# Performance work log

Measured on AMD Instinct MI355X. Metric: run time of the kernel, lower is better.

The kernel has to match this reference:

```python
import jax, jax.numpy as jnp
import numpy as np

# dims: batch, history P, horizon Q, hidden D, nodes N, cells C=H*W, Z channels
B_, P_, Q_, D_, N_, C_, H_, W_, CZ = 16, 12, 12, 64, 2000, 1024, 32, 32, 2
K_DIFF = 3  # max diffusion step of DCGRUCell -> K+1 Chebyshev terms


def _mlp2(x, w1, b1, w2, b2):
    return jax.nn.relu(x @ w1 + b1) @ w2 + b2


def _st_embedding(SE, TE, sw1, sb1, sw2, sb2, tw1, tb1, tw2, tb2):
    # GMAN-style spatio-temporal embedding: SE (M,D), TE (B,P,2) ints
    se = _mlp2(SE, sw1, sb1, sw2, sb2)                                  # (M, D)
    te = jnp.concatenate([jax.nn.one_hot(TE[..., 0], 7, dtype=SE.dtype),
                          jax.nn.one_hot(TE[..., 1], 288, dtype=SE.dtype)], axis=-1)
    te = _mlp2(te, tw1, tb1, tw2, tb2)                                  # (B, P, D)
    return se[None, None] + te[:, :, None, :]                           # (B, P, M, D)


def _scaled_laplacian(adj):
    # DCRNN 'laplacian' filter: L_tilde = 2 L / lambda_max - I, lambda_max ~= 2
    A = jnp.maximum(adj, adj.T)
    d = A.sum(axis=1)
    dinv = jnp.where(d > 0, jax.lax.rsqrt(d), 0.0)
    eye = jnp.eye(A.shape[0], dtype=A.dtype)
    L = eye - (dinv[:, None] * A) * dinv[None, :]
    return L - eye


def _gconv(x, L, K):
    # Chebyshev diffusion features: x (B,N,F) -> (B,N,F*(K+1))
    xs = [x, jnp.einsum('nm,bmf->bnf', L, x)]
    for _ in range(2, K + 1):
        xs.append(2.0 * jnp.einsum('nm,bmf->bnf', L, xs[-1]) - xs[-2])
    b, n, f = x.shape
    return jnp.stack(xs, axis=-1).reshape(b, n, f * (K + 1))


def _hard_sigmoid(x):
    return jnp.clip(0.2 * x + 0.5, 0.0, 1.0)


def _conv2d(x, w):
    return jax.lax.conv_general_dilated(x, w, (1, 1), 'SAME',
        dimension_numbers=('NHWC', 'HWIO', 'NHWC'))


def _forward(X, Z, TE, adj_gg, adj_gr, gumbel_noise, se_x, se_z, movement_logits,
             stex_se_w1, stex_se_b1, stex_se_w2, stex_se_b2,
             stex_te_w1, stex_te_b1, stex_te_w2, stex_te_b2,
             stez_se_w1, stez_se_b1, stez_se_w2, stez_se_b2,
             stez_te_w1, stez_te_b1, stez_te_w2, stez_te_b2,
             fcs_z_w1, fcs_z_b1, fcs_z_w2, fcs_z_b2,
             fcs_x_in_w1, fcs_x_in_b1, fcs_x_in_w2, fcs_x_in_b2,
             mov_fc_w, mov_fc_b,
             fcs_x_out_w1, fcs_x_out_b1, fcs_x_out_w2, fcs_x_out_b2,
             convlstm_wx, convlstm_wh,
             dcgru_gate_w, dcgru_gate_b, dcgru_cand_w, dcgru_cand_b):
    B = X.shape[0]
    TEp = TE.astype(jnp.int32)[:, :P_, :]
    # --- cell branch ---
    STEZ = _st_embedding(se_z, TEp, stez_se_w1, stez_se_b1, stez_se_w2, stez_se_b2,
                         stez_te_w1, stez_te_b1, stez_te_w2, stez_te_b2)
    Zf = _mlp2(Z, fcs_z_w1, fcs_z_b1, fcs_z_w2, fcs_z_b2) + STEZ          # (B,P,C,D)
    Zg = Zf.reshape(B, P_, H_, W_, D_)
    def clstm_step(carry, x):
        h, c = carry
        gates = _conv2d(x, convlstm_wx) + _conv2d(h, convlstm_wh)         # (B,H,W,4D)
        i, f, g, o = jnp.split(gates, 4, axis=-1)
        c = _hard_sigmoid(f) * c + _hard_sigmoid(i) * jnp.tanh(g)
        h = _hard_sigmoid(o) * jnp.tanh(c)
        return (h, c), h
    hc0 = (jnp.zeros((B, H_, W_, D_), X.dtype), jnp.zeros((B, H_, W_, D_), X.dtype))
    _, hs = jax.lax.scan(clstm_step, hc0, jnp.swapaxes(Zg, 0, 1))
    Zc = jnp.swapaxes(hs, 0, 1).reshape(B, P_, C_, D_)
    # gumbel-softmax routing over cells (soft, tau=1)
    g = -jnp.log(-jnp.log(gumbel_noise + 1e-20) + 1e-20)
    mZ = jax.nn.softmax(movement_logits + g, axis=-1)                     # (C,C)
    Zc = jnp.einsum('cd,bpdk->bpck', mZ, Zc)
    Zc = jax.nn.relu(Zc @ mov_fc_w + mov_fc_b)
    ZX = jnp.einsum('nc,bpck->bpnk', adj_gr, Zc)                          # (B,P,N,D)
    # --- node branch ---
    STEX = _st_embedding(se_x, TEp, stex_se_w1, stex_se_b1, stex_se_w2, stex_se_b2,
                         stex_te_w1, stex_te_b1, stex_te_w2, stex_te_b2)
    Xf = _mlp2(X[..., None], fcs_x_in_w1, fcs_x_in_b1, fcs_x_in_w2, fcs_x_in_b2) + STEX + ZX
    L = _scaled_laplacian(adj_gg)
    def dcgru_step(h, x):
        xh = jnp.concatenate([x, h], axis=-1)                             # (B,N,2D)
        ru = jax.nn.sigmoid(_gconv(xh, L, K_DIFF) @ dcgru_gate_w + dcgru_gate_b)
        r, u = jnp.split(ru, 2, axis=-1)
        cnd = jnp.tanh(_gconv(jnp.concatenate([x, r * h], axis=-1), L, K_DIFF)
                       @ dcgru_cand_w + dcgru_cand_b)
        return u * h + (1.0 - u) * cnd, None
    h_last, _ = jax.lax.scan(dcgru_step, jnp.zeros((B, N_, D_), X.dtype),
                             jnp.swapaxes(Xf, 0, 1))                      # (B,N,D)
    Y = _mlp2(h_last, fcs_x_out_w1, fcs_x_out_b1, fcs_x_out_w2, fcs_x_out_b2)  # (B,N,Q)
    return jnp.transpose(Y, (0, 2, 1))                                    # (B,Q,N)


def setup_inputs() -> dict:
    key = jax.random.key(0)
    ks = iter(jax.random.split(key, 64))
    def rn(shape, s=0.05):
        return jax.random.normal(next(ks), shape, dtype=jnp.float32) * s
    def ru(shape):
        return jax.random.uniform(next(ks), shape, dtype=jnp.float32)
    z = lambda *s: jnp.zeros(s, jnp.float32)
    NM = K_DIFF + 1
    inp = {
        'X': rn((B_, P_, N_), 1.0),
        'Z': rn((B_, P_, C_, CZ), 1.0),
        'TE': jax.random.randint(next(ks), (B_, P_ + Q_, 2), 0, 7, dtype=jnp.int32),
        'adj_gg': ru((N_, N_)),
        'adj_gr': ru((N_, C_)) * 0.01,
        'gumbel_noise': jnp.clip(ru((C_, C_)), 1e-6, 1.0 - 1e-6),
        'se_x': rn((N_, D_)), 'se_z': rn((C_, D_)),
        'movement_logits': rn((C_, C_)),
        'stex_se_w1': rn((D_, D_)), 'stex_se_b1': z(D_), 'stex_se_w2': rn((D_, D_)), 'stex_se_b2': z(D_),
        'stex_te_w1': rn((295, D_)), 'stex_te_b1': z(D_), 'stex_te_w2': rn((D_, D_)), 'stex_te_b2': z(D_),
        'stez_se_w1': rn((D_, D_)), 'stez_se_b1': z(D_), 'stez_se_w2': rn((D_, D_)), 'stez_se_b2': z(D_),
        'stez_te_w1': rn((295, D_)), 'stez_te_b1': z(D_), 'stez_te_w2': rn((D_, D_)), 'stez_te_b2': z(D_),
        'fcs_z_w1': rn((CZ, D_)), 'fcs_z_b1': z(D_), 'fcs_z_w2': rn((D_, D_)), 'fcs_z_b2': z(D_),
        'fcs_x_in_w1': rn((1, D_)), 'fcs_x_in_b1': z(D_), 'fcs_x_in_w2': rn((D_, D_)), 'fcs_x_in_b2': z(D_),
        'mov_fc_w': rn((D_, D_)), 'mov_fc_b': z(D_),
        'fcs_x_out_w1': rn((D_, D_)), 'fcs_x_out_b1': z(D_), 'fcs_x_out_w2': rn((D_, Q_)), 'fcs_x_out_b2': z(Q_),
        'convlstm_wx': rn((3, 3, D_, 4 * D_)), 'convlstm_wh': rn((3, 3, D_, 4 * D_)),
        'dcgru_gate_w': rn((2 * D_ * NM, 2 * D_)), 'dcgru_gate_b': z(2 * D_),
        'dcgru_cand_w': rn((2 * D_ * NM, D_)), 'dcgru_cand_b': z(D_),
    }
    return inp


def reference(X, Z, TE, adj_gg, adj_gr, gumbel_noise, se_x, se_z, movement_logits,
              stex_se_w1, stex_se_b1, stex_se_w2, stex_se_b2,
              stex_te_w1, stex_te_b1, stex_te_w2, stex_te_b2,
              stez_se_w1, stez_se_b1, stez_se_w2, stez_se_b2,
              stez_te_w1, stez_te_b1, stez_te_w2, stez_te_b2,
              fcs_z_w1, fcs_z_b1, fcs_z_w2, fcs_z_b2,
              fcs_x_in_w1, fcs_x_in_b1, fcs_x_in_w2, fcs_x_in_b2,
              mov_fc_w, mov_fc_b,
              fcs_x_out_w1, fcs_x_out_b1, fcs_x_out_w2, fcs_x_out_b2,
              convlstm_wx, convlstm_wh,
              dcgru_gate_w, dcgru_gate_b, dcgru_cand_w, dcgru_cand_b):
    return _forward(X, Z, TE, adj_gg, adj_gr, gumbel_noise, se_x, se_z, movement_logits,
                    stex_se_w1, stex_se_b1, stex_se_w2, stex_se_b2,
                    stex_te_w1, stex_te_b1, stex_te_w2, stex_te_b2,
                    stez_se_w1, stez_se_b1, stez_se_w2, stez_se_b2,
                    stez_te_w1, stez_te_b1, stez_te_w2, stez_te_b2,
                    fcs_z_w1, fcs_z_b1, fcs_z_w2, fcs_z_b2,
                    fcs_x_in_w1, fcs_x_in_b1, fcs_x_in_w2, fcs_x_in_b2,
                    mov_fc_w, mov_fc_b,
                    fcs_x_out_w1, fcs_x_out_b1, fcs_x_out_w2, fcs_x_out_b2,
                    convlstm_wx, convlstm_wh,
                    dcgru_gate_w, dcgru_gate_b, dcgru_cand_w, dcgru_cand_b)
```

## Files before the change

kernel.cpp:

```cpp
#include <hip/hip_runtime.h>
#include <hip/hip_bf16.h>
#include <math.h>

typedef _Float16 fp16;
typedef _Float16 f16x8 __attribute__((ext_vector_type(8)));
typedef float f32x4 __attribute__((ext_vector_type(4)));

#define BB 16
#define PP 12
#define QQ 12
#define NN 2000
#define CC 1024
#define GP 34
#define GP2 1156

static __device__ __forceinline__ float ldf(float v) { return v; }
static __device__ __forceinline__ float ldf(fp16 v) { return (float)v; }
static __device__ __forceinline__ void stf(float* p, float v) { *p = v; }
static __device__ __forceinline__ void stf(fp16* p, float v) { *p = (fp16)v; }

static __device__ __forceinline__ void gload_lds16(const fp16* g, fp16* l) {
  __builtin_amdgcn_global_load_lds(
      (const __attribute__((address_space(1))) void*)g,
      (__attribute__((address_space(3))) void*)l, 16, 0, 0);
}


__global__ void k_f2h(fp16* __restrict__ dst, const float* __restrict__ src, long long n) {
  long long i = (long long)blockIdx.x * 256 + threadIdx.x;
  if (i < n) dst[i] = (fp16)src[i];
}

__global__ void k_wcatT(fp16* __restrict__ dst, const float* __restrict__ w39,
                        const float* __restrict__ w40) {
  int i = blockIdx.x * 256 + threadIdx.x;
  if (i >= 1152 * 256) return;
  int n = i & 255, kk = i >> 8;
  float v = (kk < 576) ? w39[kk * 256 + n] : w40[(kk - 576) * 256 + n];
  dst[(long long)n * 1152 + kk] = (fp16)v;
}

__global__ void k_gru_repackT(fp16* __restrict__ dst, const float* __restrict__ src, int O) {
  int i = blockIdx.x * 256 + threadIdx.x;
  if (i >= O * 512) return;
  int d = i >> 9;
  int kc = i & 511;
  int t = kc >> 7;
  int c = kc & 127;
  dst[i] = (fp16)src[(c * 4 + t) * O + d];
}

__global__ void k_w2T(fp16* __restrict__ dst, const float* __restrict__ src) {
  int i = blockIdx.x * 256 + threadIdx.x;
  if (i >= 4096) return;
  int d = i >> 6, k = i & 63;
  dst[i] = (fp16)src[k * 64 + d];
}

__global__ void k_dinv(const float* __restrict__ adj, float* __restrict__ dinv) {
  int row = blockIdx.x;
  float s = 0.f;
  for (int j = threadIdx.x; j < NN; j += 256)
    s += fmaxf(adj[(long long)row * NN + j], adj[(long long)j * NN + row]);
  __shared__ float red[256];
  red[threadIdx.x] = s;
  __syncthreads();
  for (int st = 128; st > 0; st >>= 1) {
    if (threadIdx.x < st) red[threadIdx.x] += red[threadIdx.x + st];
    __syncthreads();
  }
  if (threadIdx.x == 0) {
    float d = red[0];
    dinv[row] = d > 0.f ? 1.0f / sqrtf(d) : 0.f;
  }
}

__global__ void k_L(const float* __restrict__ adj, const float* __restrict__ dinv,
                    fp16* __restrict__ Lh) {
  long long i = (long long)blockIdx.x * 256 + threadIdx.x;
  if (i >= (long long)NN * NN) return;
  int r = (int)(i / NN), c = (int)(i % NN);
  float a = fmaxf(adj[(long long)r * NN + c], adj[(long long)c * NN + r]);
  Lh[(long long)r * 2048 + c] = (fp16)(-dinv[r] * a * dinv[c]);
}

__global__ void k_subdiag(fp16* __restrict__ M2) {
  int i = blockIdx.x * 256 + threadIdx.x;
  if (i >= NN) return;
  M2[(long long)i * 2048 + i] = (fp16)((float)M2[(long long)i * 2048 + i] - 1.0f);
}

__global__ void k_gumbel_softmax(const float* __restrict__ ml, const float* __restrict__ gn,
                                 fp16* __restrict__ mZ) {
  int row = blockIdx.x;
  __shared__ float buf[CC];
  __shared__ float red[256];
  int t = threadIdx.x;
  float mx = -1e30f;
  for (int j = t; j < CC; j += 256) {
    float u = gn[(long long)row * CC + j];
    float g = -logf(-logf(u + 1e-20f) + 1e-20f);
    float v = ml[(long long)row * CC + j] + g;
    buf[j] = v;
    mx = fmaxf(mx, v);
  }
  red[t] = mx;
  __syncthreads();
  for (int st = 128; st > 0; st >>= 1) {
    if (t < st) red[t] = fmaxf(red[t], red[t + st]);
    __syncthreads();
  }
  mx = red[0];
  __syncthreads();
  float s = 0.f;
  for (int j = t; j < CC; j += 256) {
    float e = expf(buf[j] - mx);
    buf[j] = e;
    s += e;
  }
  red[t] = s;
  __syncthreads();
  for (int st = 128; st > 0; st >>= 1) {
    if (t < st) red[t] += red[t + st];
    __syncthreads();
  }
  float inv = 1.0f / red[0];
  for (int j = t; j < CC; j += 256) mZ[(long long)row * CC + j] = (fp16)(buf[j] * inv);
}

__global__ void k_te(const int* __restrict__ TE, const float* __restrict__ w1,
                     const float* __restrict__ b1, float* __restrict__ tmp) {
  int i = blockIdx.x * 256 + threadIdx.x;
  if (i >= BB * PP * 64) return;
  int j = i & 63;
  int bp = i >> 6;
  int b = bp / PP, p = bp % PP;
  int te0 = TE[(b * (PP + QQ) + p) * 2 + 0];
  int te1 = TE[(b * (PP + QQ) + p) * 2 + 1];
  float v = w1[te0 * 64 + j] + w1[(7 + te1) * 64 + j] + b1[j];
  tmp[i] = fmaxf(v, 0.f);
}

__global__ void k_addb(float* __restrict__ dst, const float* __restrict__ b, int n) {
  int i = blockIdx.x * 256 + threadIdx.x;
  if (i < n) dst[i] += b[i & 63];
}

__global__ void k_zf1(const float* __restrict__ Z, const float* __restrict__ w1,
                      const float* __restrict__ b1, fp16* __restrict__ tmp) {
  long long i = (long long)blockIdx.x * 256 + threadIdx.x;
  if (i >= (long long)BB * PP * CC * 64) return;
  int j = (int)(i & 63);
  long long row = i >> 6;
  float v = Z[row * 2 + 0] * w1[j] + Z[row * 2 + 1] * w1[64 + j] + b1[j];
  tmp[i] = (fp16)fmaxf(v, 0.f);
}

__global__ void k_add_stez(fp16* __restrict__ dst, const fp16* __restrict__ src,
                           const float* __restrict__ seZ, const float* __restrict__ teZ) {
  long long i = (long long)blockIdx.x * 256 + threadIdx.x;
  if (i >= (long long)BB * PP * CC * 64) return;
  int j = (int)(i & 63);
  long long row = i >> 6;
  int c = (int)(row & 1023);
  int bp = (int)(row >> 10);
  int pc = ((c >> 5) + 1) * GP + (c & 31) + 1;
  dst[((long long)bp * GP2 + pc) * 64 + j] =
      (fp16)((float)src[i] + seZ[c * 64 + j] + teZ[bp * 64 + j]);
}

template <typename TA, typename TB, typename TC>
__global__ __launch_bounds__(256) void gemm_t(
    const TA* __restrict__ A, int lda, long long sA,
    const TB* __restrict__ Bm, int ldb, long long sB,
    TC* Cm, int ldc, long long sC,
    const TC* S, long long sS,
    const float* __restrict__ bias,
    int M, int Ncols, int K, float alpha, float beta, int act) {
  int bz = blockIdx.z;
  A += (long long)bz * sA;
  Bm += (long long)bz * sB;
  Cm += (long long)bz * sC;
  if (S) S += (long long)bz * sS;
  const int row0 = blockIdx.x * 64, col0 = blockIdx.y * 64;
  __shared__ float As[16][68];
  __shared__ float Bs[16][68];
  int tid = threadIdx.x, tx = tid & 15, ty = tid >> 4;
  float acc[4][4] = {};
  for (int k0 = 0; k0 < K; k0 += 16) {
#pragma unroll
    for (int j = 0; j < 4; ++j) {
      int e = tid + 256 * j;
      int m = e >> 4, kk = e & 15;
      int gm = row0 + m;
      As[kk][m] = (gm < M) ? ldf(A[(long long)gm * lda + k0 + kk]) : 0.f;
    }
#pragma unroll
    for (int j = 0; j < 4; ++j) {
      int e = tid + 256 * j;
      int kk = e >> 6, n = e & 63;
      int gn = col0 + n;
      Bs[kk][n] = (gn < Ncols) ? ldf(Bm[(long long)(k0 + kk) * ldb + gn]) : 0.f;
    }
    __syncthreads();
#pragma unroll
    for (int kk = 0; kk < 16; ++kk) {
      float a[4], bb[4];
#pragma unroll
      for (int i = 0; i < 4; ++i) a[i] = As[kk][ty * 4 + i];
#pragma unroll
      for (int j = 0; j < 4; ++j) bb[j] = Bs[kk][tx * 4 + j];
#pragma unroll
      for (int i = 0; i < 4; ++i)
#pragma unroll
        for (int j = 0; j < 4; ++j) acc[i][j] = fmaf(a[i], bb[j], acc[i][j]);
    }
    __syncthreads();
  }
#pragma unroll
  for (int i = 0; i < 4; ++i) {
    int r = row0 + ty * 4 + i;
    if (r >= M) continue;
#pragma unroll
    for (int j = 0; j < 4; ++j) {
      int cn = col0 + tx * 4 + j;
      if (cn >= Ncols) continue;
      float v = alpha * acc[i][j];
      if (bias) v += bias[cn];
      if (S) v += beta * ldf(S[(long long)r * ldc + cn]);
      if (act == 1) v = fmaxf(v, 0.f);
      else if (act == 2) v = 1.f / (1.f + expf(-v));
      else if (act == 3) v = tanhf(v);
      stf(&Cm[(long long)r * ldc + cn], v);
    }
  }
}

template <int MT, int MODE>
__global__ __launch_bounds__(256) void mfma7(
    const fp16* __restrict__ A,
    const fp16* __restrict__ U0base, long long uZ, int bHi,
    const fp16* __restrict__ xB, long long xZ,
    const fp16* __restrict__ Xc, long long XcSlab, int Xcld, int Xczmul,
    const fp16* __restrict__ Hc, long long HcSlab, int Hcld, int Hczmul,
    fp16* __restrict__ C, int ldc, long long cBatch,
    const float* __restrict__ bias,
    fp16* __restrict__ rhOut, const fp16* __restrict__ hIn,
    const fp16* __restrict__ uIn, long long uStride,
    int M, int Ncols) {
  __shared__ fp16 As[2][MT * 32];
  __shared__ fp16 Bs[2][64 * 32];
  const int z = blockIdx.z;
  const int n0 = blockIdx.y * 64;
  const fp16* U0z = U0base + (long long)z * uZ;
  const fp16* xBz = xB + (long long)z * xZ;
  C += (long long)z * cBatch;
  if (rhOut) rhOut += (long long)z * uZ;
  if (hIn) hIn += (long long)z * uZ;
  if (uIn) uIn += (long long)z * uStride;
  const int tid = threadIdx.x;
  const int lane = tid & 63, wv = tid >> 6;
  const int wr = wv >> 1, wc = wv & 1;
  const int quad = lane >> 4, ln = lane & 15;
  constexpr int WM = MT / 32;

  const fp16* aSrc[MT / 64];
#pragma unroll
  for (int i = 0; i < MT / 64; ++i) {
    int c = i * 256 + tid;
    int row = c >> 2;
    int lseg = (c & 3) ^ ((c >> 3) & 3);
    aSrc[i] = A + (long long)row * 512 + lseg * 8;
  }
  const int brow = tid >> 2;
  const int blseg = (tid & 3) ^ ((tid >> 3) & 3);
  const long long bnode = n0 + brow;

  f32x4 acc[WM][2];
#pragma unroll
  for (int i = 0; i < WM; ++i)
#pragma unroll
    for (int j = 0; j < 2; ++j) acc[i][j] = (f32x4){0.f, 0.f, 0.f, 0.f};

  auto stage = [&](int t, int buf) {
    const int k0 = t * 32;
#pragma unroll
    for (int i = 0; i < MT / 64; ++i)
      gload_lds16(aSrc[i] + k0, &As[buf][(i * 256 + tid) * 8]);
    if (k0 < 128) {
      int kin = k0 + (tid & 31);
      int ngrp = tid >> 5;
      int n = n0 + ngrp * 8;
      const fp16* src = (kin < 64) ? (xBz + (long long)kin * 2048 + n)
                                   : (U0z + (long long)(kin + bHi) * 2048 + n);
      f16x8 v = *(const f16x8*)src;
      int kk = tid & 31;
#pragma unroll
      for (int j = 0; j < 8; ++j) {
        int rn = ngrp * 8 + j;
        Bs[buf][rn * 32 + ((((kk >> 3) ^ ((rn >> 1) & 3)) << 3) | (kk & 7))] = v[j];
      }
    } else {
      int slab = k0 >> 7;
      int kin = (k0 & 127) + blseg * 8;
      const fp16* src;
      if (kin < 64)
        src = Xc + (long long)(slab - 1) * XcSlab + bnode * Xcld +
              (long long)z * Xczmul + kin;
      else
        src = Hc + (long long)(slab - 1) * HcSlab + bnode * Hcld +
              (long long)z * Hczmul + (kin - 64);
      gload_lds16(src, &Bs[buf][tid * 8]);
    }
  };

  const int sw = (quad ^ ((ln >> 1) & 3)) << 3;
  stage(0, 0);
  for (int t = 0; t < 16; ++t) {
    const int buf = t & 1;
    __syncthreads();
    if (t + 1 < 16) stage(t + 1, buf ^ 1);
    f16x8 af[WM], bf[2];
#pragma unroll
    for (int wm = 0; wm < WM; ++wm) {
      int row = wr * (MT / 2) + wm * 16 + ln;
      af[wm] = *(const f16x8*)&As[buf][row * 32 + sw];
    }
#pragma unroll
    for (int wn = 0; wn < 2; ++wn) {
      int row = wc * 32 + wn * 16 + ln;
      bf[wn] = *(const f16x8*)&Bs[buf][row * 32 + sw];
    }
#pragma unroll
    for (int wm = 0; wm < WM; ++wm)
#pragma unroll
      for (int wn = 0; wn < 2; ++wn)
        acc[wm][wn] =
            __builtin_amdgcn_mfma_f32_16x16x32_f16(af[wm], bf[wn], acc[wm][wn], 0, 0, 0);
  }
#pragma unroll
  for (int wm = 0; wm < WM; ++wm) {
#pragma unroll
    for (int wn = 0; wn < 2; ++wn) {
#pragma unroll
      for (int r = 0; r < 4; ++r) {
        int gm = wr * (MT / 2) + wm * 16 + quad * 4 + r;
        int gn = n0 + wc * 32 + wn * 16 + ln;
        if (gm < M && gn < Ncols) {
          float v = acc[wm][wn][r];
          v += bias[gm];
          if (MODE == 1) {
            v = 1.f / (1.f + expf(-v));
            C[(long long)gm * ldc + gn] = (fp16)v;
            if (gm < 64) {
              float h = (float)hIn[(long long)gm * 2048 + gn];
              rhOut[(long long)gm * 2048 + gn] = (fp16)(v * h);
            }
          } else {
            v = tanhf(v);
            float u = (float)uIn[(long long)(64 + gm) * NN + gn];
            long long ci = (long long)gm * ldc + gn;
            float h = (float)C[ci];
            C[ci] = (fp16)(u * h + (1.f - u) * v);
          }
        }
      }
    }
  }
}

template <int MT, int NT>
__global__ __launch_bounds__(256) void mfma3(
    const fp16* __restrict__ A, int lda, long long zA, int aMsh, long long aMslab,
    const fp16* __restrict__ B, int ldb, long long zB,
    fp16* __restrict__ C, int ldc, long long zC, int cMsh, long long cMslab, int cNsh,
    long long cNslab,
    const fp16* __restrict__ S, long long zS, float beta,
    const float* __restrict__ rowBias, long long zRB,
    const float* __restrict__ s2T, int s2ld,
    int M, int Ncols, int K, float alpha, int act) {
  __shared__ fp16 As[MT][40];
  __shared__ fp16 Bs[NT][40];
  const int z = blockIdx.z;
  const int gm0 = blockIdx.x * MT, n0 = blockIdx.y * NT;
  A += (long long)z * zA;
  B += (long long)z * zB;
  C += (long long)z * zC;
  if (S) S += (long long)z * zS;
  const int tid = threadIdx.x;
  const int lane = tid & 63, wv = tid >> 6;
  const int wr = wv >> 1, wc = wv & 1;
  const int quad = lane >> 4, ln = lane & 15;
  const unsigned aMmask = (1u << aMsh) - 1u;
  const unsigned cMmask = (1u << cMsh) - 1u;
  const unsigned cNmask = (1u << cNsh) - 1u;
  constexpr int WM = MT / 32, WN = NT / 32;
  f32x4 acc[WM][WN];
#pragma unroll
  for (int i = 0; i < WM; ++i)
#pragma unroll
    for (int j = 0; j < WN; ++j) acc[i][j] = (f32x4){0.f, 0.f, 0.f, 0.f};

  for (int k0 = 0; k0 < K; k0 += 32) {
#pragma unroll
    for (int i = 0; i < MT / 64; ++i) {
      int c = tid + 256 * i;
      int row = c >> 2, seg = c & 3;
      int gm = gm0 + row;
      int kk0 = k0 + seg * 8;
      const fp16* src = A + ((long long)((unsigned)gm >> aMsh)) * aMslab +
                        (long long)(gm & aMmask) * lda + kk0;
      if (gm < M && kk0 + 8 <= K) {
        *(f16x8*)&As[row][seg * 8] = *(const f16x8*)src;
      } else {
#pragma unroll
        for (int j = 0; j < 8; ++j)
          As[row][seg * 8 + j] = (gm < M && kk0 + j < K) ? src[j] : (fp16)0.f;
      }
    }
#pragma unroll
    for (int i = 0; i < NT / 64; ++i) {
      int c = tid + 256 * i;
      int n = c >> 2, seg = c & 3;
      int gn = n0 + n;
      int kk0 = k0 + seg * 8;
      const fp16* src = B + (long long)gn * ldb + kk0;
      if (gn < Ncols && kk0 + 8 <= K) {
        *(f16x8*)&Bs[n][seg * 8] = *(const f16x8*)src;
      } else {
#pragma unroll
        for (int j = 0; j < 8; ++j)
          Bs[n][seg * 8 + j] = (gn < Ncols && kk0 + j < K) ? src[j] : (fp16)0.f;
      }
    }
    __syncthreads();
    f16x8 af[WM], bf[WN];
#pragma unroll
    for (int wm = 0; wm < WM; ++wm)
      af[wm] = *(const f16x8*)&As[wr * (MT / 2) + wm * 16 + ln][quad * 8];
#pragma unroll
    for (int wn = 0; wn < WN; ++wn)
      bf[wn] = *(const f16x8*)&Bs[wc * (NT / 2) + wn * 16 + ln][quad * 8];
#pragma unroll
    for (int wm = 0; wm < WM; ++wm)
#pragma unroll
      for (int wn = 0; wn < WN; ++wn)
        acc[wm][wn] =
            __builtin_amdgcn_mfma_f32_16x16x32_f16(af[wm], bf[wn], acc[wm][wn], 0, 0, 0);
    __syncthreads();
  }
#pragma unroll
  for (int wm = 0; wm < WM; ++wm) {
#pragma unroll
    for (int wn = 0; wn < WN; ++wn) {
#pragma unroll
      for (int r = 0; r < 4; ++r) {
        int gm = gm0 + wr * (MT / 2) + wm * 16 + quad * 4 + r;
        int gn = n0 + wc * (NT / 2) + wn * 16 + ln;
        if (gm < M && gn < Ncols) {
          float v = alpha * acc[wm][wn][r];
          if (rowBias) v += rowBias[(long long)z * zRB + gm];
          if (s2T) v += s2T[(long long)gn * s2ld + gm];
          long long ci = ((long long)((unsigned)gm >> cMsh)) * cMslab +
                         (long long)(gm & cMmask) * ldc +
                         ((long long)((unsigned)gn >> cNsh)) * cNslab + (gn & cNmask);
          if (S) v += beta * (float)S[ci];
          if (act == 1) v = fmaxf(v, 0.f);
          else if (act == 2) v = 1.f / (1.f + expf(-v));
          else if (act == 3) v = tanhf(v);
          C[ci] = (fp16)v;
        }
// ... 84 lines not shown
      int row = wc * (NT / 2) + wn * 16 + ln;
      bf[wn] = *(const f16x8*)&Bs[buf][row * 32 + sw];
    }
#pragma unroll
    for (int wm = 0; wm < WM; ++wm)
#pragma unroll
      for (int wn = 0; wn < WN; ++wn)
        acc[wm][wn] =
            __builtin_amdgcn_mfma_f32_16x16x32_f16(af[wm], bf[wn], acc[wm][wn], 0, 0, 0);
  }
#pragma unroll
  for (int wm = 0; wm < WM; ++wm)
#pragma unroll
    for (int wn = 0; wn < WN; ++wn)
#pragma unroll
      for (int r = 0; r < 4; ++r) {
        int gm = gm0 + wr * (MT / 2) + wm * 16 + quad * 4 + r;
        int gn = n0 + wc * (NT / 2) + wn * 16 + ln;
        long long ci = ((long long)((unsigned)gm >> cMsh)) * cMslab +
                       (long long)(gm & cMmask) * ldc +
                       ((long long)((unsigned)gn >> cNsh)) * cNslab + (gn & cNmask);
        float v = alpha * acc[wm][wn][r];
        if (S) v += beta * (float)S[ci];
        C[ci] = (fp16)v;
      }
}

template <int MT, int NT>
__global__ __launch_bounds__(256) void mfma6(
    const fp16* __restrict__ A, int lda,
    const fp16* __restrict__ b0, const fp16* __restrict__ b1, int rsh, int ssh,
    long long z0, long long z1, int ldb,
    fp16* __restrict__ C, int ldc, int cMsh, long long cMslab,
    int K) {
  __shared__ fp16 As[2][MT * 32];
  __shared__ fp16 Bs[2][NT * 32];
  const int tid = threadIdx.x;
  const int gm0 = blockIdx.x * MT, n0 = blockIdx.y * NT;
  const unsigned cMmask = (1u << cMsh) - 1u;
  const int lane = tid & 63, wv = tid >> 6;
  const int wr = wv >> 1, wc = wv & 1;
  const int quad = lane >> 4, ln = lane & 15;
  constexpr int WM = MT / 32, WN = NT / 32;

  const fp16* aSrc[MT / 64];
  const fp16* bSrc[NT / 64];
#pragma unroll
  for (int i = 0; i < MT / 64; ++i) {
    int c = i * 256 + tid;
    int lseg = (c & 3) ^ ((c >> 3) & 3);
    aSrc[i] = A + (long long)(gm0 + (c >> 2)) * lda + lseg * 8;
  }
#pragma unroll
  for (int i = 0; i < NT / 64; ++i) {
    int c = i * 256 + tid;
    int lseg = (c & 3) ^ ((c >> 3) & 3);
    int gn = n0 + (c >> 2);
    unsigned b = (unsigned)gn >> rsh;
    unsigned wi = (unsigned)gn & ((1u << rsh) - 1u);
    unsigned sel = wi >> ssh;
    unsigned r = wi & ((1u << ssh) - 1u);
    const fp16* bb = sel ? (b1 + (long long)b * z1) : (b0 + (long long)b * z0);
    bSrc[i] = bb + (long long)r * ldb + lseg * 8;
  }

  f32x4 acc[WM][WN];
#pragma unroll
  for (int i = 0; i < WM; ++i)
#pragma unroll
    for (int j = 0; j < WN; ++j) acc[i][j] = (f32x4){0.f, 0.f, 0.f, 0.f};

  const int sw = (quad ^ ((ln >> 1) & 3)) << 3;

#pragma unroll
  for (int i = 0; i < MT / 64; ++i) gload_lds16(aSrc[i], &As[0][(i * 256 + tid) * 8]);
#pragma unroll
  for (int i = 0; i < NT / 64; ++i) gload_lds16(bSrc[i], &Bs[0][(i * 256 + tid) * 8]);

  const int nk = K >> 5;
  for (int t = 0; t < nk; ++t) {
    const int buf = t & 1;
    __syncthreads();
    if (t + 1 < nk) {
      const int k1 = (t + 1) * 32;
#pragma unroll
      for (int i = 0; i < MT / 64; ++i)
        gload_lds16(aSrc[i] + k1, &As[buf ^ 1][(i * 256 + tid) * 8]);
#pragma unroll
      for (int i = 0; i < NT / 64; ++i)
        gload_lds16(bSrc[i] + k1, &Bs[buf ^ 1][(i * 256 + tid) * 8]);
    }
    f16x8 af[WM], bf[WN];
#pragma unroll
    for (int wm = 0; wm < WM; ++wm) {
      int row = wr * (MT / 2) + wm * 16 + ln;
      af[wm] = *(const f16x8*)&As[buf][row * 32 + sw];
    }
#pragma unroll
    for (int wn = 0; wn < WN; ++wn) {
      int row = wc * (NT / 2) + wn * 16 + ln;
      bf[wn] = *(const f16x8*)&Bs[buf][row * 32 + sw];
    }
#pragma unroll
    for (int wm = 0; wm < WM; ++wm)
#pragma unroll
      for (int wn = 0; wn < WN; ++wn)
        acc[wm][wn] =
            __builtin_amdgcn_mfma_f32_16x16x32_f16(af[wm], bf[wn], acc[wm][wn], 0, 0, 0);
  }
#pragma unroll
  for (int wm = 0; wm < WM; ++wm)
#pragma unroll
    for (int wn = 0; wn < WN; ++wn)
#pragma unroll
      for (int r = 0; r < 4; ++r) {
        int gm = gm0 + wr * (MT / 2) + wm * 16 + quad * 4 + r;
        int gn = n0 + wc * (NT / 2) + wn * 16 + ln;
        long long ci = ((long long)((unsigned)gm >> cMsh)) * cMslab +
                       (long long)(gm & cMmask) * ldc + gn;
        C[ci] = (fp16)acc[wm][wn][r];
      }
}

__global__ __launch_bounds__(256) void k_zxtfin(
    const fp16* __restrict__ w2T, const fp16* __restrict__ Tmat,
    fp16* __restrict__ ZXt, const float* __restrict__ teXb, const float* __restrict__ seX) {
  __shared__ fp16 As[64][72];
  __shared__ fp16 Bs[128][72];
  const int z = blockIdx.z;
  const int n0 = blockIdx.y * 128;
  const fp16* Tz = Tmat + (long long)z * 2048 * 64;
  fp16* Cz = ZXt + (long long)z * 64 * 2048;
  const float* tb = teXb + z * 64;
  const int tid = threadIdx.x;
  const int lane = tid & 63, wv = tid >> 6;
  const int wr = wv >> 1, wc = wv & 1;
  const int quad = lane >> 4, ln = lane & 15;
#pragma unroll
  for (int i = 0; i < 2; ++i) {
    int c = tid + 256 * i;
    int row = c >> 3, seg = c & 7;
    *(f16x8*)&As[row][seg * 8] = *(const f16x8*)(w2T + row * 64 + seg * 8);
  }
#pragma unroll
  for (int i = 0; i < 4; ++i) {
    int c = tid + 256 * i;
    int row = c >> 3, seg = c & 7;
    *(f16x8*)&Bs[row][seg * 8] =
        *(const f16x8*)(Tz + (long long)(n0 + row) * 64 + seg * 8);
  }
  __syncthreads();
  f32x4 acc[2][4];
#pragma unroll
  for (int i = 0; i < 2; ++i)
#pragma unroll
    for (int j = 0; j < 4; ++j) acc[i][j] = (f32x4){0.f, 0.f, 0.f, 0.f};
#pragma unroll
  for (int kt = 0; kt < 2; ++kt) {
    f16x8 af[2], bf[4];
#pragma unroll
    for (int wm = 0; wm < 2; ++wm)
      af[wm] = *(const f16x8*)&As[wr * 32 + wm * 16 + ln][kt * 32 + quad * 8];
#pragma unroll
    for (int wn = 0; wn < 4; ++wn)
      bf[wn] = *(const f16x8*)&Bs[wc * 64 + wn * 16 + ln][kt * 32 + quad * 8];
#pragma unroll
    for (int wm = 0; wm < 2; ++wm)
#pragma unroll
      for (int wn = 0; wn < 4; ++wn)
        acc[wm][wn] =
            __builtin_amdgcn_mfma_f32_16x16x32_f16(af[wm], bf[wn], acc[wm][wn], 0, 0, 0);
  }
#pragma unroll
  for (int wm = 0; wm < 2; ++wm)
#pragma unroll
    for (int wn = 0; wn < 4; ++wn)
#pragma unroll
      for (int r = 0; r < 4; ++r) {
        int gm = wr * 32 + wm * 16 + quad * 4 + r;
        int gn = n0 + wc * 64 + wn * 16 + ln;
        long long ci = (long long)gm * 2048 + gn;
        float v = 0.f;
        if (gn < NN)
          v = acc[wm][wn][r] + (float)Cz[ci] + tb[gm] + seX[(long long)gn * 64 + gm];
        Cz[ci] = (fp16)v;
      }
}

__global__ __launch_bounds__(256) void k_conv4(
    const fp16* __restrict__ Zfp, const fp16* __restrict__ hp,
    const fp16* __restrict__ wcatT, fp16* __restrict__ gates, int p) {
  __shared__ fp16 As[2][128 * 32];
  __shared__ fp16 Bs[2][64 * 32];
  const int gm0 = blockIdx.x * 128, n0 = blockIdx.y * 64;
  const int tid = threadIdx.x;
  const int lane = tid & 63, wv = tid >> 6;
  const int wr = wv >> 1, wc = wv & 1;
  const int quad = lane >> 4, ln = lane & 15;

  long long aZ[2], aH[2];
#pragma unroll
  for (int i = 0; i < 2; ++i) {
    int c = tid + 256 * i;
    int row = c >> 2;
    int lseg = (c & 3) ^ ((c >> 3) & 3);
    int m = gm0 + row;
    int b = m >> 10, y = (m >> 5) & 31, x = m & 31;
    int pc = (y + 1) * GP + (x + 1);
    aZ[i] = ((long long)(b * PP + p) * GP2 + pc) * 64 + lseg * 8;
    aH[i] = ((long long)b * GP2 + pc) * 64 + lseg * 8;
  }
  const fp16* bBase;
  {
    int row = tid >> 2;
    int lseg = (tid & 3) ^ ((tid >> 3) & 3);
    bBase = wcatT + (long long)(n0 + row) * 1152 + lseg * 8;
  }
  f32x4 acc[4][2];
#pragma unroll
  for (int i = 0; i < 4; ++i)
#pragma unroll
    for (int j = 0; j < 2; ++j) acc[i][j] = (f32x4){0.f, 0.f, 0.f, 0.f};

  auto stage = [&](int t, int buf) {
    int tap = (t >> 1) % 9, half = t & 1;
    int srcsel = t >= 18;
    int off = ((tap / 3 - 1) * GP + (tap % 3 - 1)) * 64 + half * 32;
#pragma unroll
    for (int i = 0; i < 2; ++i) {
      const fp16* src = srcsel ? (hp + aH[i] + off) : (Zfp + aZ[i] + off);
      gload_lds16(src, &As[buf][(i * 256 + tid) * 8]);
    }
    gload_lds16(bBase + t * 32, &Bs[buf][tid * 8]);
  };
  stage(0, 0);
  const int sw = (quad ^ ((ln >> 1) & 3)) << 3;
  for (int t = 0; t < 36; ++t) {
    const int buf = t & 1;
    __syncthreads();
    if (t + 1 < 36) stage(t + 1, buf ^ 1);
    f16x8 af[4], bf[2];
#pragma unroll
    for (int wm = 0; wm < 4; ++wm) {
      int row = wr * 64 + wm * 16 + ln;
      af[wm] = *(const f16x8*)&As[buf][row * 32 + sw];
    }
#pragma unroll
    for (int wn = 0; wn < 2; ++wn) {
      int row = wc * 32 + wn * 16 + ln;
      bf[wn] = *(const f16x8*)&Bs[buf][row * 32 + sw];
    }
#pragma unroll
    for (int wm = 0; wm < 4; ++wm)
#pragma unroll
      for (int wn = 0; wn < 2; ++wn)
        acc[wm][wn] =
            __builtin_amdgcn_mfma_f32_16x16x32_f16(af[wm], bf[wn], acc[wm][wn], 0, 0, 0);
  }
#pragma unroll
  for (int wm = 0; wm < 4; ++wm)
#pragma unroll
    for (int wn = 0; wn < 2; ++wn)
#pragma unroll
      for (int r = 0; r < 4; ++r) {
        int gm = gm0 + wr * 64 + wm * 16 + quad * 4 + r;
        int gn = n0 + wc * 32 + wn * 16 + ln;
        gates[(long long)gm * 256 + gn] = (fp16)acc[wm][wn][r];
      }
}

__global__ void k_clstm_update(const fp16* __restrict__ gates, float* __restrict__ c,
                               fp16* __restrict__ h, fp16* __restrict__ ZclT, int p) {
  long long i = (long long)blockIdx.x * 256 + threadIdx.x;
  if (i >= (long long)BB * CC * 64) return;
  int d = (int)(i & 63);
  long long bc = i >> 6;
  int b = (int)(bc >> 10);
  int cell = (int)(bc & 1023);
  const fp16* g = gates + (((long long)b * CC) + cell) * 256;
  float gi = (float)g[d], gf = (float)g[64 + d], gg = (float)g[128 + d],
        go = (float)g[192 + d];
  float hs_f = fminf(fmaxf(0.2f * gf + 0.5f, 0.f), 1.f);
  float hs_i = fminf(fmaxf(0.2f * gi + 0.5f, 0.f), 1.f);
  float hs_o = fminf(fmaxf(0.2f * go + 0.5f, 0.f), 1.f);
  float cv = hs_f * c[i] + hs_i * tanhf(gg);
  c[i] = cv;
  float hv = hs_o * tanhf(cv);
  int pc = ((cell >> 5) + 1) * GP + (cell & 31) + 1;
  h[((long long)b * GP2 + pc) * 64 + d] = (fp16)hv;
  ZclT[(((long long)(b * PP + p)) * 64 + d) * CC + cell] = (fp16)hv;
}

__global__ void k_tmat(const float* __restrict__ X, const float* __restrict__ w1,
                       const float* __restrict__ b1, fp16* __restrict__ T, long long nrows) {
  long long i = (long long)blockIdx.x * 256 + threadIdx.x;
  if (i >= nrows * 64) return;
  int j = (int)(i & 63);
  long long row = i >> 6;
  int z = (int)(row / NN);
  int n = (int)(row - (long long)z * NN);
  T[(((long long)z * 2048) + n) * 64 + j] = (fp16)fmaxf(X[row] * w1[j] + b1[j], 0.f);
}

__global__ void k_trT(const fp16* __restrict__ U0, float* __restrict__ htmp) {
  long long i = (long long)blockIdx.x * 256 + threadIdx.x;
  if (i >= (long long)BB * NN * 64) return;
  int d = (int)(i & 63);
  long long bn = i >> 6;
  int b = (int)(bn / NN);
  int n = (int)(bn % NN);
  htmp[i] = (float)U0[((long long)b * 192 + 64 + d) * 2048 + n];
}

__global__ void k_out(const float* __restrict__ Y, float* __restrict__ out) {
  int i = blockIdx.x * 256 + threadIdx.x;
  if (i >= BB * QQ * NN) return;
  int n = i % NN;
  int bq = i / NN;
  int b = bq / QQ, q = bq % QQ;
  out[i] = Y[((long long)b * NN + n) * 12 + q];
}

template <typename TA, typename TB, typename TC>
static void launch_gemm(hipStream_t stream, const TA* A, int lda, long long sA,
                        const TB* Bm, int ldb, long long sB, TC* Cm, int ldc, long long sC,
                        const TC* S, long long sS, const float* bias, int M, int Nc, int K,
                        float alpha, float beta, int act, int batch) {
  dim3 g((M + 63) / 64, (Nc + 63) / 64, batch);
  gemm_t<TA, TB, TC><<<g, dim3(256), 0, stream>>>(A, lda, sA, Bm, ldb, sB, Cm, ldc, sC, S,
                                                  sS, bias, M, Nc, K, alpha, beta, act);
}

extern "C" void kernel_launch(void* const* d_in, const int* in_sizes, int n_in,
                              void* d_out, int out_size, void* d_ws, size_t ws_size,
                              hipStream_t stream) {
  char* base = (char*)d_ws;
  size_t off = 0;
  auto alloc_bytes = [&](size_t nb) -> char* {
    char* p = base + off;
    off += (nb + 255) & ~(size_t)255;
    return p;
  };
  auto allocf = [&](size_t n) -> float* { return (float*)alloc_bytes(n * 4); };
  auto alloch = [&](size_t n) -> fp16* { return (fp16*)alloc_bytes(n * 2); };

  const float* X = (const float*)d_in[0];
  const float* Z = (const float*)d_in[1];
  const int* TE = (const int*)d_in[2];
  const float* adj_gg = (const float*)d_in[3];
  const float* adj_gr = (const float*)d_in[4];
  const float* gumbel = (const float*)d_in[5];
  const float* se_x = (const float*)d_in[6];
  const float* se_z = (const float*)d_in[7];
  const float* movement = (const float*)d_in[8];
  auto W = [&](int i) { return (const float*)d_in[i]; };

  fp16* wcatT = alloch((size_t)256 * 1152);
  fp16* gwT = alloch(128 * 512);
  fp16* cwT = alloch(64 * 512);
  fp16* w2T = alloch(64 * 64);
  fp16* w2mT = alloch(64 * 64);
  float* dinv = allocf(NN);
  fp16* LMall = alloch((size_t)6144 * 2048);
  fp16* mZh = alloch((size_t)CC * CC);
  fp16* agh2 = alloch((size_t)2048 * CC);
  float* seZ = allocf(CC * 64);
  float* teZ = allocf(BB * PP * 64);
  float* seX = allocf(NN * 64);
  float* teXb = allocf(BB * PP * 64);
  float* mtmp = allocf(NN * 64);
  float* tetmp = allocf(BB * PP * 64);
  fp16* ruT = alloch((size_t)BB * 128 * NN);
  char* pool = alloc_bytes(50331648);
  fp16* Uall = (fp16*)pool;
  fp16* gates = (fp16*)pool;
  fp16* chh = (fp16*)(pool + 8388608);
  float* ccc = (float*)(pool + 12582912);
  fp16* Zmix = (fp16*)pool;
  fp16* ZmovT = (fp16*)(pool + 25165824);
  fp16* zpool = alloch((size_t)BB * PP * 64 * 2048);
  fp16* Zfp = zpool;
  fp16* ZXt = zpool;
  fp16* Zc = alloch((size_t)BB * PP * CC * 64);

  if (off > ws_size) return;

  const long long uB = 192LL * 2048;
  const long long USL = 16LL * uB;
  const long long ZXB = 12LL * 64 * 2048;
  fp16* Lh = LMall;
  fp16* M2h = LMall + 2048LL * 2048;
  fp16* M3h = LMall + 4096LL * 2048;
  const int KCH = 2016;

  k_wcatT<<<dim3(1152), dim3(256), 0, stream>>>(wcatT, W(39), W(40));
  k_gru_repackT<<<dim3(256), dim3(256), 0, stream>>>(gwT, W(41), 128);
  k_gru_repackT<<<dim3(128), dim3(256), 0, stream>>>(cwT, W(43), 64);
  k_w2T<<<dim3(16), dim3(256), 0, stream>>>(w2T, W(31));
  k_w2T<<<dim3(16), dim3(256), 0, stream>>>(w2mT, W(33));
  k_dinv<<<dim3(NN), dim3(256), 0, stream>>>(adj_gg, dinv);
  hipMemsetAsync(LMall, 0, (size_t)6144 * 2048 * 2, stream);
  k_L<<<dim3((NN * NN + 255) / 256), dim3(256), 0, stream>>>(adj_gg, dinv, Lh);
  mfma4<64, 128><<<dim3(32, 16, 1), dim3(256), 0, stream>>>(
      Lh, Lh, 31, 31, 0LL, 0LL, 2048, Lh, 2048, 0LL, M2h, 2048, 0LL, 31, 0LL, 31, 0LL,
      (const fp16*)nullptr, 2.f, 0.f, KCH);
  k_subdiag<<<dim3((NN + 255) / 256), dim3(256), 0, stream>>>(M2h);
  mfma4<64, 128><<<dim3(32, 16, 1), dim3(256), 0, stream>>>(
      Lh, Lh, 31, 31, 0LL, 0LL, 2048, M2h, 2048, 0LL, M3h, 2048, 0LL, 31, 0LL, 31, 0LL,
      (const fp16*)Lh, 2.f, -1.f, KCH);
  k_gumbel_softmax<<<dim3(CC), dim3(256), 0, stream>>>(movement, gumbel, mZh);
  k_f2h<<<dim3((NN * CC + 255) / 256), dim3(256), 0, stream>>>(agh2, adj_gr,
                                                               (long long)NN * CC);
  hipMemsetAsync(agh2 + (size_t)NN * CC, 0, (size_t)(2048 - NN) * CC * 2, stream);

  launch_gemm(stream, se_z, 64, 0LL, W(17), 64, 0LL, mtmp, 64, 0LL, (float*)nullptr, 0LL,
              W(18), CC, 64, 64, 1.f, 0.f, 1, 1);
  launch_gemm(stream, (const float*)mtmp, 64, 0LL, W(19), 64, 0LL, seZ, 64, 0LL,
              (float*)nullptr, 0LL, W(20), CC, 64, 64, 1.f, 0.f, 0, 1);
  k_te<<<dim3((BB * PP * 64 + 255) / 256), dim3(256), 0, stream>>>(TE, W(21), W(22), tetmp);
  launch_gemm(stream, (const float*)tetmp, 64, 0LL, W(23), 64, 0LL, teZ, 64, 0LL,
              (float*)nullptr, 0LL, W(24), BB * PP, 64, 64, 1.f, 0.f, 0, 1);
  launch_gemm(stream, se_x, 64, 0LL, W(9), 64, 0LL, mtmp, 64, 0LL, (float*)nullptr, 0LL,
              W(10), NN, 64, 64, 1.f, 0.f, 1, 1);
  launch_gemm(stream, (const float*)mtmp, 64, 0LL, W(11), 64, 0LL, seX, 64, 0LL,
              (float*)nullptr, 0LL, W(12), NN, 64, 64, 1.f, 0.f, 0, 1);
  k_te<<<dim3((BB * PP * 64 + 255) / 256), dim3(256), 0, stream>>>(TE, W(13), W(14), tetmp);
  launch_gemm(stream, (const float*)tetmp, 64, 0LL, W(15), 64, 0LL, teXb, 64, 0LL,
              (float*)nullptr, 0LL, W(16), BB * PP, 64, 64, 1.f, 0.f, 0, 1);
  k_addb<<<dim3((BB * PP * 64 + 255) / 256), dim3(256), 0, stream>>>(teXb, W(32),
                                                                     BB * PP * 64);

  long long nZ = (long long)BB * PP * CC * 64;
  k_zf1<<<dim3((int)((nZ + 255) / 256)), dim3(256), 0, stream>>>(Z, W(25), W(26), Zc);
  launch_gemm(stream, (const fp16*)Zc, 64, 0LL, W(27), 64, 0LL, (fp16*)pool, 64, 0LL,
              (fp16*)nullptr, 0LL, W(28), BB * PP * CC, 64, 64, 1.f, 0.f, 0, 1);
  hipMemsetAsync(zpool, 0, (size_t)BB * PP * GP2 * 64 * 2, stream);
  k_add_stez<<<dim3((int)((nZ + 255) / 256)), dim3(256), 0, stream>>>(Zfp, (fp16*)pool,
                                                                      seZ, teZ);

  hipMemsetAsync(chh, 0, (size_t)BB * GP2 * 64 * 2, stream);
  hipMemsetAsync(ccc, 0, (size_t)BB * CC * 64 * 4, stream);
  for (int p = 0; p < PP; ++p) {
    k_conv4<<<dim3(BB * CC / 128, 4), dim3(256), 0, stream>>>(Zfp, chh, wcatT, gates, p);
    k_clstm_update<<<dim3((int)(((long long)BB * CC * 64 + 255) / 256)), dim3(256), 0,
                     stream>>>(gates, ccc, chh, Zc, p);
  }

  mfma4<128, 64><<<dim3(8, 1, 192), dim3(256), 0, stream>>>(
      mZh, mZh, 31, 31, 0LL, 0LL, CC, (const fp16*)Zc, CC, (long long)64 * CC, Zmix, 64,
      (long long)CC * 64, 31, 0LL, 31, 0LL, (const fp16*)nullptr, 1.f, 0.f, CC);
  mfma3<64, 128><<<dim3(1, 8, 192), dim3(256), 0, stream>>>(
      w2mT, 64, 0LL, 31, 0LL, Zmix, 64, (long long)CC * 64, ZmovT, CC, (long long)64 * CC,
      31, 0LL, 31, 0LL, (const fp16*)nullptr, 0LL, 0.f, W(34), 0LL, nullptr, 0, 64, CC, 64,
      1.f, 1);

  mfma4<128, 128><<<dim3(96, 16, 1), dim3(256), 0, stream>>>(
      ZmovT, ZmovT, 31, 31, 0LL, 0LL, 1024, agh2, 1024, 0LL, ZXt, 2048, 0LL, 31, 0LL, 31,
      0LL, (const fp16*)nullptr, 1.f, 0.f, 1024);

  fp16* Tmat = Zc;
  for (int half = 0; half < 2; ++half) {
    long long z0 = 96LL * half;
    k_tmat<<<dim3((int)((96LL * NN * 64 + 255) / 256)), dim3(256), 0, stream>>>(
        X + z0 * NN, W(29), W(30), Tmat, 96LL * NN);
    k_zxtfin<<<dim3(1, 16, 96), dim3(256), 0, stream>>>(
        w2T, Tmat, ZXt + z0 * 64 * 2048, teXb + z0 * 64, seX);
  }

  fp16* U0 = Uall;
  fp16* Tn = Uall + USL;
  fp16* Tn2 = Uall + 3 * USL;
  const long long TnSlab = 2048LL * 2048;
  const long long Tn2Slab = 2048LL * 1024;
  hipMemsetAsync(U0, 0, (size_t)USL * 2, stream);

  for (int p = 0; p < PP; ++p) {
    const fp16* xP = ZXt + (long long)p * 64 * 2048;
    mfma6<128, 128><<<dim3(48, 16), dim3(256), 0, stream>>>(
        LMall, 2048, xP, U0 + 64 * 2048, 7, 6, ZXB, uB, 2048, Tn, 2048, 11, TnSlab, KCH);
    mfma7<128, 1><<<dim3(1, 32, BB), dim3(256), 0, stream>>>(
        gwT, U0, uB, 0, xP, ZXB,
        Tn, TnSlab, 2048, 128,
        Tn + 64, TnSlab, 2048, 128,
        ruT, NN, (long long)128 * NN, W(42), U0 + 128 * 2048, U0 + 64 * 2048,
        (const fp16*)nullptr, 0LL, 128, NN);
    mfma6<128, 128><<<dim3(48, 8), dim3(256), 0, stream>>>(
        LMall, 2048, U0 + 128 * 2048, U0 + 128 * 2048, 6, 6, uB, uB, 2048, Tn2, 1024, 11,
        Tn2Slab, KCH);
    mfma7<64, 2><<<dim3(1, 32, BB), dim3(256), 0, stream>>>(
        cwT, U0, uB, 64, xP, ZXB,
        Tn, TnSlab, 2048, 128,
        Tn2, Tn2Slab, 1024, 64,
        U0 + 64 * 2048, 2048, uB, W(44), (fp16*)nullptr, (const fp16*)nullptr,
        (const fp16*)ruT, (long long)128 * NN, 64, NN);
  }

  float* htmp = (float*)Zc;
  float* out1 = (float*)(Zc + 5120000);
  float* out2 = (float*)(Zc + 10240000);
  k_trT<<<dim3((int)(((long long)BB * NN * 64 + 255) / 256)), dim3(256), 0, stream>>>(U0,
                                                                                      htmp);
  launch_gemm(stream, (const float*)htmp, 64, 0LL, W(35), 64, 0LL, out1, 64, 0LL,
              (float*)nullptr, 0LL, W(36), BB * NN, 64, 64, 1.f, 0.f, 1, 1);
  launch_gemm(stream, (const float*)out1, 64, 0LL, W(37), 12, 0LL, out2, 12, 0LL,
              (float*)nullptr, 0LL, W(38), BB * NN, 12, 64, 1.f, 0.f, 0, 1);
  k_out<<<dim3((BB * QQ * NN + 255) / 256), dim3(256), 0, stream>>>(out2, (float*)d_out);
}
```

Before: 2.938 ms.

## Fuse Z second MLP layer with ST-embedding scatter and fuse output head into MFMA kernel

Result: no change. 2.908 ms (-1.0%).

```diff
diff --git a/kernel.cpp b/kernel.cpp
--- a/kernel.cpp
+++ b/kernel.cpp
@@ -55,6 +55,13 @@
   if (i >= 4096) return;
   int d = i >> 6, k = i & 63;
   dst[i] = (fp16)src[k * 64 + d];
+}
+
+__global__ void k_wT(fp16* __restrict__ dst, const float* __restrict__ src, int J, int JP) {
+  int i = blockIdx.x * 256 + threadIdx.x;
+  if (i >= JP * 64) return;
+  int j = i >> 6, k = i & 63;
+  dst[i] = (fp16)((j < J) ? src[k * J + j] : 0.f);
 }
 
 __global__ void k_dinv(const float* __restrict__ adj, float* __restrict__ dinv) {
@@ -156,17 +163,165 @@
   tmp[i] = (fp16)fmaxf(v, 0.f);
 }
 
-__global__ void k_add_stez(fp16* __restrict__ dst, const fp16* __restrict__ src,
-                           const float* __restrict__ seZ, const float* __restrict__ teZ) {
-  long long i = (long long)blockIdx.x * 256 + threadIdx.x;
-  if (i >= (long long)BB * PP * CC * 64) return;
-  int j = (int)(i & 63);
-  long long row = i >> 6;
-  int c = (int)(row & 1023);
-  int bp = (int)(row >> 10);
-  int pc = ((c >> 5) + 1) * GP + (c & 31) + 1;
-  dst[((long long)bp * GP2 + pc) * 64 + j] =
-      (fp16)((float)src[i] + seZ[c * 64 + j] + teZ[bp * 64 + j]);
+__global__ __launch_bounds__(256) void k_zf2(
+    const fp16* __restrict__ A, const fp16* __restrict__ w27T,
+    const float* __restrict__ b28, const float* __restrict__ seZ,
+    const float* __restrict__ teZ, fp16* __restrict__ Zfp) {
+  __shared__ fp16 As[128 * 64];
+  __shared__ fp16 Bs[64 * 64];
+  const int tid = threadIdx.x;
+  const int gm0 = blockIdx.x * 128;
+  const int lane = tid & 63, wv = tid >> 6;
+  const int wr = wv >> 1, wc = wv & 1;
+  const int quad = lane >> 4, ln = lane & 15;
+#pragma unroll
+  for (int i = 0; i < 4; ++i) {
+    int c = i * 256 + tid;
+    int row = c >> 3;
+    int lseg = (c & 7) ^ (row & 7);
+    gload_lds16(A + (long long)(gm0 + row) * 64 + lseg * 8, &As[c * 8]);
+  }
+#pragma unroll
+  for (int i = 0; i < 2; ++i) {
+    int c = i * 256 + tid;
+    int row = c >> 3;
+    int lseg = (c & 7) ^ (row & 7);
+    gload_lds16(w27T + (long long)row * 64 + lseg * 8, &Bs[c * 8]);
+  }
+  f32x4 acc[4][2];
+#pragma unroll
+  for (int i = 0; i < 4; ++i)
+#pragma unroll
+    for (int j = 0; j < 2; ++j) acc[i][j] = (f32x4){0.f, 0.f, 0.f, 0.f};
+  __syncthreads();
+#pragma unroll
+  for (int kt = 0; kt < 2; ++kt) {
+    f16x8 af[4], bf[2];
+#pragma unroll
+    for (int wm = 0; wm < 4; ++wm) {
+      int row = wr * 64 + wm * 16 + ln;
+      int slot = (kt * 4 + quad) ^ (row & 7);
+      af[wm] = *(const f16x8*)&As[row * 64 + slot * 8];
+    }
+#pragma unroll
+    for (int wn = 0; wn < 2; ++wn) {
+      int row = wc * 32 + wn * 16 + ln;
+      int slot = (kt * 4 + quad) ^ (row & 7);
+      bf[wn] = *(const f16x8*)&Bs[row * 64 + slot * 8];
+    }
+#pragma unroll
+    for (int wm = 0; wm < 4; ++wm)
+#pragma unroll
+      for (int wn = 0; wn < 2; ++wn)
+        acc[wm][wn] =
+            __builtin_amdgcn_mfma_f32_16x16x32_f16(af[wm], bf[wn], acc[wm][wn], 0, 0, 0);
+  }
+#pragma unroll
+  for (int wm = 0; wm < 4; ++wm)
+#pragma unroll
+    for (int wn = 0; wn < 2; ++wn)
+#pragma unroll
+      for (int r = 0; r < 4; ++r) {
+        int gm = gm0 + wr * 64 + wm * 16 + quad * 4 + r;
+        int j = wc * 32 + wn * 16 + ln;
+        int c = gm & 1023;
+        int bp = gm >> 10;
+        int pc = ((c >> 5) + 1) * GP + (c & 31) + 1;
+        Zfp[((long long)bp * GP2 + pc) * 64 + j] =
+            (fp16)(acc[wm][wn][r] + b28[j] + seZ[c * 64 + j] + teZ[bp * 64 + j]);
+      }
+}
+
+__global__ __launch_bounds__(256) void k_head(
+    const fp16* __restrict__ U0, const fp16* __restrict__ w35T,
+    const float* __restrict__ b36, const fp16* __restrict__ w37T,
+    const float* __restrict__ b38, float* __restrict__ out) {
+  __shared__ fp16 hT[128 * 72];
+  __shared__ fp16 Bs[64 * 64];
+  __shared__ fp16 h2[128 * 72];
+  const int b = blockIdx.y;
+  const int n0 = blockIdx.x * 128;
+  const int tid = threadIdx.x;
+  const int lane = tid & 63, wv = tid >> 6;
+  const int wr = wv >> 1, wc = wv & 1;
+  const int quad = lane >> 4, ln = lane & 15;
+  const fp16* hbase = U0 + ((long long)b * 192 + 64) * 2048;
+#pragma unroll
+  for (int i = 0; i < 4; ++i) {
+    int task = i * 256 + tid;
+    int d = task >> 4, ng = task & 15;
+    f16x8 v = *(const f16x8*)(hbase + (long long)d * 2048 + n0 + ng * 8);
+#pragma unroll
+    for (int k = 0; k < 8; ++k) hT[(ng * 8 + k) * 72 + d] = v[k];
+  }
+#pragma unroll
+  for (int i = 0; i < 2; ++i) {
+    int c = i * 256 + tid;
+    int row = c >> 3, s = c & 7;
+    *(f16x8*)&Bs[row * 64 + (s ^ (row & 7)) * 8] =
+        *(const f16x8*)(w35T + row * 64 + s * 8);
+  }
+  __syncthreads();
+  f32x4 a1[4][2];
+#pragma unroll
+  for (int i = 0; i < 4; ++i)
+#pragma unroll
+    for (int j = 0; j < 2; ++j) a1[i][j] = (f32x4){0.f, 0.f, 0.f, 0.f};
+#pragma unroll
+  for (int kt = 0; kt < 2; ++kt) {
+    f16x8 af[4], bf[2];
+#pragma unroll
+    for (int wm = 0; wm < 4; ++wm) {
+      int row = wr * 64 + wm * 16 + ln;
+      af[wm] = *(const f16x8*)&hT[row * 72 + kt * 32 + quad * 8];
+    }
+#pragma unroll
+    for (int wn = 0; wn < 2; ++wn) {
+      int row = wc * 32 + wn * 16 + ln;
+      int slot = (kt * 4 + quad) ^ (row & 7);
+      bf[wn] = *(const f16x8*)&Bs[row * 64 + slot * 8];
+    }
+#pragma unroll
+    for (int wm = 0; wm < 4; ++wm)
+#pragma unroll
+      for (int wn = 0; wn < 2; ++wn)
+        a1[wm][wn] =
+            __builtin_amdgcn_mfma_f32_16x16x32_f16(af[wm], bf[wn], a1[wm][wn], 0, 0, 0);
+  }
+#pragma unroll
+  for (int wm = 0; wm < 4; ++wm)
+#pragma unroll
+    for (int wn = 0; wn < 2; ++wn)
+#pragma unroll
+      for (int r = 0; r < 4; ++r) {
+        int rl = wr * 64 + wm * 16 + quad * 4 + r;
+        int j = wc * 32 + wn * 16 + ln;
+        h2[rl * 72 + j] = (fp16)fmaxf(a1[wm][wn][r] + b36[j], 0.f);
+      }
+  __syncthreads();
+  f32x4 a2[2];
+#pragma unroll
+  for (int i = 0; i < 2; ++i) a2[i] = (f32x4){0.f, 0.f, 0.f, 0.f};
+#pragma unroll
+  for (int kt = 0; kt < 2; ++kt) {
+    f16x8 bf = *(const f16x8*)(w37T + ln * 64 + kt * 32 + quad * 8);
+#pragma unroll
+    for (int wm = 0; wm < 2; ++wm) {
+      int row = wv * 32 + wm * 16 + ln;
+      f16x8 af = *(const f16x8*)&h2[row * 72 + kt * 32 + quad * 8];
+      a2[wm] = __builtin_amdgcn_mfma_f32_16x16x32_f16(af, bf, a2[wm], 0, 0, 0);
+    }
+  }
+#pragma unroll
+  for (int wm = 0; wm < 2; ++wm)
+#pragma unroll
+    for (int r = 0; r < 4; ++r) {
+      int nl = wv * 32 + wm * 16 + quad * 4 + r;
+      int n = n0 + nl;
+      int q = ln;
+      if (n < NN && q < 12)
+        out[((long long)b * 12 + q) * NN + n] = a2[wm][r] + b38[q];
+    }
 }
 
 template <typename TA, typename TB, typename TC>
@@ -857,25 +1012,6 @@
   T[(((long long)z * 2048) + n) * 64 + j] = (fp16)fmaxf(X[row] * w1[j] + b1[j], 0.f);
 }
 
-__global__ void k_trT(const fp16* __restrict__ U0, float* __restrict__ htmp) {
-  long long i = (long long)blockIdx.x * 256 + threadIdx.x;
-  if (i >= (long long)BB * NN * 64) return;
-  int d = (int)(i & 63);
-  long long bn = i >> 6;
-  int b = (int)(bn / NN);
-  int n = (int)(bn % NN);
-  htmp[i] = (float)U0[((long long)b * 192 + 64 + d) * 2048 + n];
-}
-
-__global__ void k_out(const float* __restrict__ Y, float* __restrict__ out) {
-  int i = blockIdx.x * 256 + threadIdx.x;
-  if (i >= BB * QQ * NN) return;
-  int n = i % NN;
-  int bq = i / NN;
-  int b = bq / QQ, q = bq % QQ;
-  out[i] = Y[((long long)b * NN + n) * 12 + q];
-}
-
 template <typename TA, typename TB, typename TC>
 static void launch_gemm(hipStream_t stream, const TA* A, int lda, long long sA,
                         const TB* Bm, int ldb, long long sB, TC* Cm, int ldc, long long sC,
@@ -915,6 +1051,9 @@
   fp16* cwT = alloch(64 * 512);
   fp16* w2T = alloch(64 * 64);
   fp16* w2mT = alloch(64 * 64);
+  fp16* w27T = alloch(64 * 64);
+  fp16* w35T = alloch(64 * 64);
+  fp16* w37T = alloch(16 * 64);
   float* dinv = allocf(NN);
   fp16* LMall = alloch((size_t)6144 * 2048);
   fp16* mZh = alloch((size_t)CC * CC);
@@ -953,6 +1092,9 @@
   k_gru_repackT<<<dim3(128), dim3(256), 0, stream>>>(cwT, W(43), 64);
   k_w2T<<<dim3(16), dim3(256), 0, stream>>>(w2T, W(31));
   k_w2T<<<dim3(16), dim3(256), 0, stream>>>(w2mT, W(33));
+  k_wT<<<dim3(16), dim3(256), 0, stream>>>(w27T, W(27), 64, 64);
+  k_wT<<<dim3(16), dim3(256), 0, stream>>>(w35T, W(35), 64, 64);
+  k_wT<<<dim3(4), dim3(256), 0, stream>>>(w37T, W(37), 12, 16);
   k_dinv<<<dim3(NN), dim3(256), 0, stream>>>(adj_gg, dinv);
   hipMemsetAsync(LMall, 0, (size_t)6144 * 2048 * 2, stream);
   k_L<<<dim3((NN * NN + 255) / 256), dim3(256), 0, stream>>>(adj_gg, dinv, Lh);
@@ -987,11 +1129,8 @@
 
   long long nZ = (long long)BB * PP * CC * 64;
   k_zf1<<<dim3((int)((nZ + 255) / 256)), dim3(256), 0, stream>>>(Z, W(25), W(26), Zc);
-  launch_gemm(stream, (const fp16*)Zc, 64, 0LL, W(27), 64, 0LL, (fp16*)pool, 64, 0LL,
-              (fp16*)nullptr, 0LL, W(28), BB * PP * CC, 64, 64, 1.f, 0.f, 0, 1);
   hipMemsetAsync(zpool, 0, (size_t)BB * PP * GP2 * 64 * 2, stream);
-  k_add_stez<<<dim3((int)((nZ + 255) / 256)), dim3(256), 0, stream>>>(Zfp, (fp16*)pool,
-                                                                      seZ, teZ);
+  k_zf2<<<dim3(1536), dim3(256), 0, stream>>>((const fp16*)Zc, w27T, W(28), seZ, teZ, Zfp);
 
   hipMemsetAsync(chh, 0, (size_t)BB * GP2 * 64 * 2, stream);
   hipMemsetAsync(ccc, 0, (size_t)BB * CC * 64 * 4, stream);
@@ -1050,14 +1189,6 @@
         (const fp16*)ruT, (long long)128 * NN, 64, NN);
   }
 
-  float* htmp = (float*)Zc;
-  float* out1 = (float*)(Zc + 5120000);
-  float* out2 = (float*)(Zc + 10240000);
-  k_trT<<<dim3((int)(((long long)BB * NN * 64 + 255) / 256)), dim3(256), 0, stream>>>(U0,
-                                                                                      htmp);
-  launch_gemm(stream, (const float*)htmp, 64, 0LL, W(35), 64, 0LL, out1, 64, 0LL,
-              (float*)nullptr, 0LL, W(36), BB * NN, 64, 64, 1.f, 0.f, 1, 1);
-  launch_gemm(stream, (const float*)out1, 64, 0LL, W(37), 12, 0LL, out2, 12, 0LL,
-              (float*)nullptr, 0LL, W(38), BB * NN, 12, 64, 1.f, 0.f, 0, 1);
-  k_out<<<dim3((BB * QQ * NN + 255) / 256), dim3(256), 0, stream>>>(out2, (float*)d_out);
-}
+  k_head<<<dim3(16, 16), dim3(256), 0, stream>>>(U0, w35T, W(36), w37T, W(38),
+                                                 (float*)d_out);
+}
```
